# Kernel tuning notes

Measured on AMD Instinct MI355X. Metric: run time of the kernel, lower is better.

Reference implementation:

```python
import jax, jax.numpy as jnp
import numpy as np

B, L, DIM = 2, 4096, 512
HEADS, KS = 8, 33
HEAD_DIM = DIM // HEADS
SCALE = HEAD_DIM ** -0.5


def setup_inputs() -> dict:
    key = jax.random.key(0)
    ks = jax.random.split(key, 5)
    s = 0.02
    return {
        "x": jax.random.normal(ks[0], (B, L, DIM), dtype=jnp.float32),
        "w_qkv": jax.random.normal(ks[1], (3 * DIM, DIM), dtype=jnp.float32) * s,
        "b_qkv": jax.random.normal(ks[2], (3 * DIM,), dtype=jnp.float32) * s,
        "w_proj": jax.random.normal(ks[3], (DIM, DIM), dtype=jnp.float32) * s,
        "b_proj": jax.random.normal(ks[4], (DIM,), dtype=jnp.float32) * s,
    }


def _na1d(q, k, v):
    # q,k,v: [B, L, H, d]. Each query i attends to KS tokens whose window
    # start is clamp(i - KS//2, 0, L-KS) (NATTEN boundary-clamped neighborhood).
    starts = jnp.clip(jnp.arange(L) - KS // 2, 0, L - KS)          # [L]
    idx = starts[:, None] + jnp.arange(KS)[None, :]                # [L, KS]
    k_g = k[:, idx]                                                # [B, L, KS, H, d]
    v_g = v[:, idx]                                                # [B, L, KS, H, d]
    scores = jnp.einsum("blhd,blkhd->bhlk", q * SCALE, k_g)        # [B, H, L, KS]
    attn = jax.nn.softmax(scores, axis=-1)
    out = jnp.einsum("bhlk,blkhd->blhd", attn, v_g)                # [B, L, H, d]
    return out


def reference(x, w_qkv, b_qkv, w_proj, b_proj):
    qkv = x @ w_qkv.T + b_qkv                                      # [B, L, 3*DIM]
    qkv = qkv.reshape(B, L, 3, HEADS, HEAD_DIM)
    q, k, v = qkv[:, :, 0], qkv[:, :, 1], qkv[:, :, 2]
    out = _na1d(q, k, v).reshape(B, L, DIM)
    return out @ w_proj.T + b_proj
```

## Files before the change

kernel.cpp:

```cpp
#include <hip/hip_runtime.h>
#include <hip/hip_bf16.h>

#define B_ 2
#define L_ 4096
#define DIM_ 512
#define HEADS_ 8
#define HDIM_ 64
#define KS_ 33

typedef __bf16 bf16;
typedef __bf16 bf16x4 __attribute__((ext_vector_type(4)));
typedef __bf16 bf16x8 __attribute__((ext_vector_type(8)));
typedef float f32x4 __attribute__((ext_vector_type(4)));

typedef __attribute__((address_space(3))) void lds_void;
typedef __attribute__((address_space(1))) const void glb_void;

__device__ __forceinline__ void async_cp16(const bf16* g, bf16* l)
{
    __builtin_amdgcn_global_load_lds((glb_void*)g, (lds_void*)l, 16, 0, 0);
}

__global__ __launch_bounds__(256)
void cvt_all(const float* __restrict__ x,  const float* __restrict__ wq,
             const float* __restrict__ bq, const float* __restrict__ wp,
             const float* __restrict__ bp,
             bf16* __restrict__ xb,  bf16* __restrict__ wqb,
             bf16* __restrict__ bqb, bf16* __restrict__ wpb,
             bf16* __restrict__ bpb)
{
    const int blk = blockIdx.x;
    const float* src; bf16* dst; int n, base;
    if (blk < 2048)       { src = x;  dst = xb;  n = 4194304; base = blk; }
    else if (blk < 2432)  { src = wq; dst = wqb; n = 786432;  base = blk - 2048; }
    else if (blk < 2560)  { src = wp; dst = wpb; n = 262144;  base = blk - 2432; }
    else if (blk == 2560) { src = bq; dst = bqb; n = 1536;    base = 0; }
    else                  { src = bp; dst = bpb; n = 512;     base = 0; }
    int i = base * 2048 + threadIdx.x * 8;
    if (i + 8 <= n) {
        float4 a = *(const float4*)(src + i);
        float4 b = *(const float4*)(src + i + 4);
        bf16x8 o;
        o[0] = (bf16)a.x; o[1] = (bf16)a.y; o[2] = (bf16)a.z; o[3] = (bf16)a.w;
        o[4] = (bf16)b.x; o[5] = (bf16)b.y; o[6] = (bf16)b.z; o[7] = (bf16)b.w;
        *(bf16x8*)(dst + i) = o;
    }
}

template <typename OutT>
__global__ __launch_bounds__(256)
void gemm_nt_bias(const bf16* __restrict__ A, const bf16* __restrict__ W,
                  const bf16* __restrict__ bias, OutT* __restrict__ C,
                  int M, int N, int K)
{
    __shared__ bf16 As[128][64];
    __shared__ bf16 Bs[128][64];

    const int tid  = threadIdx.x;
    const int wave = tid >> 6;
    const int lane = tid & 63;
    const int wm   = (wave >> 1) * 64;
    const int wn   = (wave & 1) * 64;
    const int l16  = lane & 15;
    const int quad = lane >> 4;

    const int row0 = blockIdx.x * 128;
    const int col0 = blockIdx.y * 128;

    f32x4 acc[4][4] = {};

    for (int k0 = 0; k0 < K; k0 += 64) {
        #pragma unroll
        for (int it = 0; it < 4; ++it) {
            int f   = it * 256 + tid;
            int r   = f >> 3;
            int c8l = (f & 7) ^ (r & 7);
            async_cp16(&A[(size_t)(row0 + r) * K + k0 + c8l * 8], &As[r][(f & 7) * 8]);
            async_cp16(&W[(size_t)(col0 + r) * K + k0 + c8l * 8], &Bs[r][(f & 7) * 8]);
        }
        __syncthreads();

        #pragma unroll
        for (int ks = 0; ks < 2; ++ks) {
            bf16x8 af[4], bfr[4];
            #pragma unroll
            for (int i = 0; i < 4; ++i) {
                int ra = wm + i * 16 + l16;
                int rb = wn + i * 16 + l16;
                af[i]  = *(const bf16x8*)(&As[ra][((ks * 4 + quad) ^ (ra & 7)) * 8]);
                bfr[i] = *(const bf16x8*)(&Bs[rb][((ks * 4 + quad) ^ (rb & 7)) * 8]);
            }
            #pragma unroll
            for (int mi = 0; mi < 4; ++mi)
                #pragma unroll
                for (int ni = 0; ni < 4; ++ni)
                    acc[mi][ni] = __builtin_amdgcn_mfma_f32_16x16x32_bf16(
                        af[mi], bfr[ni], acc[mi][ni], 0, 0, 0);
        }
        __syncthreads();
    }

    #pragma unroll
    for (int ni = 0; ni < 4; ++ni) {
        int n = col0 + wn + ni * 16 + l16;
        float bv = (float)bias[n];
        #pragma unroll
        for (int mi = 0; mi < 4; ++mi) {
            int mrow = row0 + wm + mi * 16 + quad * 4;
            #pragma unroll
            for (int r = 0; r < 4; ++r)
                C[(size_t)(mrow + r) * N + n] = (OutT)(acc[mi][ni][r] + bv);
        }
    }
}

__global__ __launch_bounds__(256)
void na1d_attn_mfma(const bf16* __restrict__ qkv, bf16* __restrict__ att)
{
    __shared__ bf16 Klds[96 * 64];
    __shared__ bf16 Vlds[96 * 66];
    __shared__ bf16 Plds[4][16][72];

    const int tid  = threadIdx.x;
    const int wave = tid >> 6;
    const int lane = tid & 63;
    const int l16  = lane & 15;
    const int quad = lane >> 4;

    const int xcd  = blockIdx.x & 7;
    const int s    = blockIdx.x >> 3;
    const int jj   = s & 3;
    const int half = (s >> 2) & 1;
    const int h    = (s >> 3) & 7;
    const int b    = s >> 6;
    const int p    = jj * 8 + xcd;
    const int Q0   = p * 128 + half * 64;

    const size_t rs = 3 * DIM_;
    const size_t rowbase = (size_t)b * L_;

    #pragma unroll
    for (int i = 0; i < 3; ++i) {
        int ck = i * 256 + tid;
        int r  = ck >> 3;
        int pc = ck & 7;
        int lc = pc ^ (r & 7);
        int g  = Q0 - 16 + r;
        g = g < 0 ? 0 : (g > L_ - 1 ? L_ - 1 : g);
        async_cp16(qkv + (rowbase + g) * rs + DIM_ + h * HDIM_ + lc * 8,
                   Klds + (size_t)ck * 8);
    }
    {
        unsigned int* V32 = (unsigned int*)Vlds;
        #pragma unroll
        for (int i = 0; i < 3; ++i) {
            int cv = i * 256 + tid;
            int r  = cv >> 3;
            int pc = cv & 7;
            int g  = Q0 - 16 + r;
            g = g < 0 ? 0 : (g > L_ - 1 ? L_ - 1 : g);
            uint4 val = *(const uint4*)(qkv + (rowbase + g) * rs + 2 * DIM_ + h * HDIM_ + pc * 8);
            int base = r * 33 + pc * 4;
            V32[base + 0] = val.x; V32[base + 1] = val.y;
            V32[base + 2] = val.z; V32[base + 3] = val.w;
        }
    }

    const int q0w = Q0 + wave * 16;
    const bf16* qptr = qkv + (rowbase + q0w + l16) * rs + h * HDIM_ + quad * 8;
    bf16x8 qf0 = *(const bf16x8*)(qptr);
    bf16x8 qf1 = *(const bf16x8*)(qptr + 32);

    int k_base = q0w - 16;
    if (k_base > L_ - 48) k_base = L_ - 48;
    if (k_base < 0) k_base = 0;
    const int rel = k_base - (Q0 - 16);

    __syncthreads();

    f32x4 sacc[3] = {};
    #pragma unroll
    for (int t = 0; t < 3; ++t) {
        int r = rel + t * 16 + l16;
        bf16x8 kf0 = *(const bf16x8*)(Klds + r * 64 + ((quad ^ (r & 7)) * 8));
        bf16x8 kf1 = *(const bf16x8*)(Klds + r * 64 + (((4 + quad) ^ (r & 7)) * 8));
        sacc[t] = __builtin_amdgcn_mfma_f32_16x16x32_bf16(qf0, kf0, sacc[t], 0, 0, 0);
        sacc[t] = __builtin_amdgcn_mfma_f32_16x16x32_bf16(qf1, kf1, sacc[t], 0, 0, 0);
    }

    int offr[4];
    #pragma unroll
    for (int r = 0; r < 4; ++r) {
        int lq = q0w + quad * 4 + r;
        int st = lq - KS_ / 2;
        if (st < 0) st = 0;
        if (st > L_ - KS_) st = L_ - KS_;
        offr[r] = st - k_base;
    }
    float sv[3][4];
    #pragma unroll
    for (int t = 0; t < 3; ++t) {
        int j = t * 16 + l16;
        #pragma unroll
        for (int r = 0; r < 4; ++r) {
            float xv = sacc[t][r] * 0.125f;
            sv[t][r] = (j >= offr[r] && j <= offr[r] + 32) ? xv : -1e30f;
        }
    }

    float mr[4], sum[4];
    #pragma unroll
    for (int r = 0; r < 4; ++r)
        mr[r] = fmaxf(fmaxf(sv[0][r], sv[1][r]), sv[2][r]);
    #pragma unroll
    for (int o = 1; o < 16; o <<= 1)
        #pragma unroll
        for (int r = 0; r < 4; ++r)
            mr[r] = fmaxf(mr[r], __shfl_xor(mr[r], o, 64));
    #pragma unroll
    for (int t = 0; t < 3; ++t)
        #pragma unroll
        for (int r = 0; r < 4; ++r)
            sv[t][r] = __expf(sv[t][r] - mr[r]);
    #pragma unroll
    for (int r = 0; r < 4; ++r)
        sum[r] = sv[0][r] + sv[1][r] + sv[2][r];
    #pragma unroll
    for (int o = 1; o < 16; o <<= 1)
        #pragma unroll
        for (int r = 0; r < 4; ++r)
            sum[r] += __shfl_xor(sum[r], o, 64);
    #pragma unroll
    for (int r = 0; r < 4; ++r) {
        float inv = 1.0f / sum[r];
        #pragma unroll
        for (int t = 0; t < 3; ++t) sv[t][r] *= inv;
    }

    bf16* P = &Plds[wave][0][0];
    {
        int rr = lane >> 2;
        int c0 = 48 + (lane & 3) * 4;
        *(bf16x4*)(&P[rr * 72 + c0]) = (bf16x4){(bf16)0.f, (bf16)0.f, (bf16)0.f, (bf16)0.f};
    }
    #pragma unroll
    for (int t = 0; t < 3; ++t)
        #pragma unroll
        for (int r = 0; r < 4; ++r)
            P[(quad * 4 + r) * 72 + t * 16 + l16] = (bf16)sv[t][r];
    __syncthreads();

    bf16x8 pf0 = *(const bf16x8*)(&P[l16 * 72 + quad * 8]);
    bf16x8 pf1 = *(const bf16x8*)(&P[l16 * 72 + 32 + quad * 8]);

    f32x4 o[4] = {};
    #pragma unroll
    for (int t = 0; t < 4; ++t) {
        bf16x8 vf0, vf1;
        #pragma unroll
        for (int j = 0; j < 8; ++j) {
            vf0[j] = Vlds[(rel + quad * 8 + j) * 66 + t * 16 + l16];
            vf1[j] = Vlds[(rel + 32 + quad * 8 + j) * 66 + t * 16 + l16];
        }
        o[t] = __builtin_amdgcn_mfma_f32_16x16x32_bf16(pf0, vf0, o[t], 0, 0, 0);
        o[t] = __builtin_amdgcn_mfma_f32_16x16x32_bf16(pf1, vf1, o[t], 0, 0, 0);
    }

    bf16* orow = att + (rowbase + q0w) * DIM_ + h * HDIM_;
    #pragma unroll
    for (int t = 0; t < 4; ++t)
        #pragma unroll
        for (int r = 0; r < 4; ++r)
            orow[(size_t)(quad * 4 + r) * DIM_ + t * 16 + l16] = (bf16)o[t][r];
}

extern "C" void kernel_launch(void* const* d_in, const int* in_sizes, int n_in,
                              void* d_out, int out_size, void* d_ws, size_t ws_size,
                              hipStream_t stream) {
    const int n_x  = B_ * L_ * DIM_;
    const int n_wq = 3 * DIM_ * DIM_;
    const int n_bq = 3 * DIM_;
    const int n_wp = DIM_ * DIM_;
    const int n_bp = DIM_;

    char* ws = (char*)d_ws;
    bf16* xb  = (bf16*)ws;
    bf16* wqb = xb  + n_x;
    bf16* bqb = wqb + n_wq;
    bf16* wpb = bqb + n_bq;
    bf16* bpb = wpb + n_wp;
    bf16* qkv = bpb + n_bp;
    bf16* att = qkv + (size_t)8192 * 1536;

    float* out = (float*)d_out;
    const int M = B_ * L_;

    cvt_all<<<2562, 256, 0, stream>>>(
        (const float*)d_in[0], (const float*)d_in[1], (const float*)d_in[2],
        (const float*)d_in[3], (const float*)d_in[4],
        xb, wqb, bqb, wpb, bpb);

    gemm_nt_bias<bf16><<<dim3(M / 128, (3 * DIM_) / 128), 256, 0, stream>>>(
        xb, wqb, bqb, qkv, M, 3 * DIM_, DIM_);

    na1d_attn_mfma<<<dim3((B_ * HEADS_ * L_) / 64), 256, 0, stream>>>(qkv, att);

    gemm_nt_bias<float><<<dim3(M / 128, DIM_ / 128), 256, 0, stream>>>(
        att, wpb, bpb, out, M, DIM_, DIM_);
}
```

Measured before the change: 123.2 us.

## Store V transposed from QKV GEMM and load V fragments directly in attention

The QKV projection now gets its own kernel that writes Q and K to a packed [M,1024] buffer and V transposed to a [B, DIM, L] buffer. The attention kernel no longer stages V through LDS with scalar 16-bit gathers. Each lane instead loads contiguous 8-element bf16 vectors of V straight from global memory as the MFMA B operand, with a clamp to stay in bounds at the sequence end. The aim is to drop the LDS transpose and the many ds_read_u16 instructions. In exchange the GEMM epilogue does strided 8-byte stores for V, and attention relies on the cache for V reuse across waves.

```diff
diff --git a/kernel.cpp b/kernel.cpp
--- a/kernel.cpp
+++ b/kernel.cpp
@@ -7,6 +7,7 @@
 #define HEADS_ 8
 #define HDIM_ 64
 #define KS_ 33
+#define QKS_ 1024
 
 typedef __bf16 bf16;
 typedef __bf16 bf16x4 __attribute__((ext_vector_type(4)));
@@ -47,11 +48,10 @@
     }
 }
 
-template <typename OutT>
 __global__ __launch_bounds__(256)
-void gemm_nt_bias(const bf16* __restrict__ A, const bf16* __restrict__ W,
-                  const bf16* __restrict__ bias, OutT* __restrict__ C,
-                  int M, int N, int K)
+void gemm_qkv(const bf16* __restrict__ A, const bf16* __restrict__ W,
+              const bf16* __restrict__ bias,
+              bf16* __restrict__ qk, bf16* __restrict__ vT)
 {
     __shared__ bf16 As[128][64];
     __shared__ bf16 Bs[128][64];
@@ -66,6 +66,7 @@
 
     const int row0 = blockIdx.x * 128;
     const int col0 = blockIdx.y * 128;
+    const int K    = DIM_;
 
     f32x4 acc[4][4] = {};
 
@@ -100,6 +101,92 @@
         __syncthreads();
     }
 
+    if (col0 < 1024) {
+        #pragma unroll
+        for (int ni = 0; ni < 4; ++ni) {
+            int n = col0 + wn + ni * 16 + l16;
+            float bv = (float)bias[n];
+            #pragma unroll
+            for (int mi = 0; mi < 4; ++mi) {
+                int mrow = row0 + wm + mi * 16 + quad * 4;
+                #pragma unroll
+                for (int r = 0; r < 4; ++r)
+                    qk[(size_t)(mrow + r) * QKS_ + n] = (bf16)(acc[mi][ni][r] + bv);
+            }
+        }
+    } else {
+        #pragma unroll
+        for (int ni = 0; ni < 4; ++ni) {
+            int nf = col0 + wn + ni * 16 + l16;
+            float bv = (float)bias[nf];
+            int hd = nf - 1024;
+            #pragma unroll
+            for (int mi = 0; mi < 4; ++mi) {
+                int m = row0 + wm + mi * 16 + quad * 4;
+                int b = m >> 12;
+                int l = m & (L_ - 1);
+                bf16x4 v4;
+                #pragma unroll
+                for (int r = 0; r < 4; ++r) v4[r] = (bf16)(acc[mi][ni][r] + bv);
+                *(bf16x4*)(vT + ((size_t)(b * DIM_ + hd)) * L_ + l) = v4;
+            }
+        }
+    }
+}
+
+template <typename OutT>
+__global__ __launch_bounds__(256)
+void gemm_nt_bias(const bf16* __restrict__ A, const bf16* __restrict__ W,
+                  const bf16* __restrict__ bias, OutT* __restrict__ C,
+                  int M, int N, int K)
+{
+    __shared__ bf16 As[128][64];
+    __shared__ bf16 Bs[128][64];
+
+    const int tid  = threadIdx.x;
+    const int wave = tid >> 6;
+    const int lane = tid & 63;
+    const int wm   = (wave >> 1) * 64;
+    const int wn   = (wave & 1) * 64;
+    const int l16  = lane & 15;
+    const int quad = lane >> 4;
+
+    const int row0 = blockIdx.x * 128;
+    const int col0 = blockIdx.y * 128;
+
+    f32x4 acc[4][4] = {};
+
+    for (int k0 = 0; k0 < K; k0 += 64) {
+        #pragma unroll
+        for (int it = 0; it < 4; ++it) {
+            int f   = it * 256 + tid;
+            int r   = f >> 3;
+            int c8l = (f & 7) ^ (r & 7);
+            async_cp16(&A[(size_t)(row0 + r) * K + k0 + c8l * 8], &As[r][(f & 7) * 8]);
+            async_cp16(&W[(size_t)(col0 + r) * K + k0 + c8l * 8], &Bs[r][(f & 7) * 8]);
+        }
+        __syncthreads();
+
+        #pragma unroll
+        for (int ks = 0; ks < 2; ++ks) {
+            bf16x8 af[4], bfr[4];
+            #pragma unroll
+            for (int i = 0; i < 4; ++i) {
+                int ra = wm + i * 16 + l16;
+                int rb = wn + i * 16 + l16;
+                af[i]  = *(const bf16x8*)(&As[ra][((ks * 4 + quad) ^ (ra & 7)) * 8]);
+                bfr[i] = *(const bf16x8*)(&Bs[rb][((ks * 4 + quad) ^ (rb & 7)) * 8]);
+            }
+            #pragma unroll
+            for (int mi = 0; mi < 4; ++mi)
+                #pragma unroll
+                for (int ni = 0; ni < 4; ++ni)
+                    acc[mi][ni] = __builtin_amdgcn_mfma_f32_16x16x32_bf16(
+                        af[mi], bfr[ni], acc[mi][ni], 0, 0, 0);
+        }
+        __syncthreads();
+    }
+
     #pragma unroll
     for (int ni = 0; ni < 4; ++ni) {
         int n = col0 + wn + ni * 16 + l16;
@@ -115,10 +202,10 @@
 }
 
 __global__ __launch_bounds__(256)
-void na1d_attn_mfma(const bf16* __restrict__ qkv, bf16* __restrict__ att)
+void na1d_attn_mfma(const bf16* __restrict__ qk, const bf16* __restrict__ vT,
+                    bf16* __restrict__ att)
 {
     __shared__ bf16 Klds[96 * 64];
-    __shared__ bf16 Vlds[96 * 66];
     __shared__ bf16 Plds[4][16][72];
 
     const int tid  = threadIdx.x;
@@ -136,7 +223,6 @@
     const int p    = jj * 8 + xcd;
     const int Q0   = p * 128 + half * 64;
 
-    const size_t rs = 3 * DIM_;
     const size_t rowbase = (size_t)b * L_;
 
     #pragma unroll
@@ -147,27 +233,12 @@
         int lc = pc ^ (r & 7);
         int g  = Q0 - 16 + r;
         g = g < 0 ? 0 : (g > L_ - 1 ? L_ - 1 : g);
-        async_cp16(qkv + (rowbase + g) * rs + DIM_ + h * HDIM_ + lc * 8,
+        async_cp16(qk + (rowbase + g) * QKS_ + DIM_ + h * HDIM_ + lc * 8,
                    Klds + (size_t)ck * 8);
     }
-    {
-        unsigned int* V32 = (unsigned int*)Vlds;
-        #pragma unroll
-        for (int i = 0; i < 3; ++i) {
-            int cv = i * 256 + tid;
-            int r  = cv >> 3;
-            int pc = cv & 7;
-            int g  = Q0 - 16 + r;
-            g = g < 0 ? 0 : (g > L_ - 1 ? L_ - 1 : g);
-            uint4 val = *(const uint4*)(qkv + (rowbase + g) * rs + 2 * DIM_ + h * HDIM_ + pc * 8);
-            int base = r * 33 + pc * 4;
-            V32[base + 0] = val.x; V32[base + 1] = val.y;
-            V32[base + 2] = val.z; V32[base + 3] = val.w;
-        }
-    }
 
     const int q0w = Q0 + wave * 16;
-    const bf16* qptr = qkv + (rowbase + q0w + l16) * rs + h * HDIM_ + quad * 8;
+    const bf16* qptr = qk + (rowbase + q0w + l16) * QKS_ + h * HDIM_ + quad * 8;
     bf16x8 qf0 = *(const bf16x8*)(qptr);
     bf16x8 qf1 = *(const bf16x8*)(qptr + 32);
 
@@ -253,15 +324,16 @@
     bf16x8 pf0 = *(const bf16x8*)(&P[l16 * 72 + quad * 8]);
     bf16x8 pf1 = *(const bf16x8*)(&P[l16 * 72 + 32 + quad * 8]);
 
+    const bf16* vbase = vT + (size_t)(b * DIM_ + h * HDIM_) * L_;
+    int c1 = k_base + quad * 8;
+    int c2 = k_base + 32 + quad * 8;
+    if (c2 > L_ - 8) c2 = L_ - 8;
     f32x4 o[4] = {};
     #pragma unroll
     for (int t = 0; t < 4; ++t) {
-        bf16x8 vf0, vf1;
-        #pragma unroll
-        for (int j = 0; j < 8; ++j) {
-            vf0[j] = Vlds[(rel + quad * 8 + j) * 66 + t * 16 + l16];
-            vf1[j] = Vlds[(rel + 32 + quad * 8 + j) * 66 + t * 16 + l16];
-        }
+        const bf16* vrow = vbase + (size_t)(t * 16 + l16) * L_;
+        bf16x8 vf0 = *(const bf16x8*)(vrow + c1);
+        bf16x8 vf1 = *(const bf16x8*)(vrow + c2);
         o[t] = __builtin_amdgcn_mfma_f32_16x16x32_bf16(pf0, vf0, o[t], 0, 0, 0);
         o[t] = __builtin_amdgcn_mfma_f32_16x16x32_bf16(pf1, vf1, o[t], 0, 0, 0);
     }
@@ -289,8 +361,9 @@
     bf16* bqb = wqb + n_wq;
     bf16* wpb = bqb + n_bq;
     bf16* bpb = wpb + n_wp;
-    bf16* qkv = bpb + n_bp;
-    bf16* att = qkv + (size_t)8192 * 1536;
+    bf16* qk  = bpb + n_bp;
+    bf16* vT  = qk  + (size_t)8192 * 1024;
+    bf16* att = vT  + (size_t)B_ * DIM_ * L_;
 
     float* out = (float*)d_out;
     const int M = B_ * L_;
@@ -300,10 +373,10 @@
         (const float*)d_in[3], (const float*)d_in[4],
         xb, wqb, bqb, wpb, bpb);
 
-    gemm_nt_bias<bf16><<<dim3(M / 128, (3 * DIM_) / 128), 256, 0, stream>>>(
-        xb, wqb, bqb, qkv, M, 3 * DIM_, DIM_);
-
-    na1d_attn_mfma<<<dim3((B_ * HEADS_ * L_) / 64), 256, 0, stream>>>(qkv, att);
+    gemm_qkv<<<dim3(M / 128, (3 * DIM_) / 128), 256, 0, stream>>>(
+        xb, wqb, bqb, qk, vT);
+
+    na1d_attn_mfma<<<dim3((B_ * HEADS_ * L_) / 64), 256, 0, stream>>>(qk, vT, att);
 
     gemm_nt_bias<float><<<dim3(M / 128, DIM_ / 128), 256, 0, stream>>>(
         att, wpb, bpb, out, M, DIM_, DIM_);
```

After: 125.3 us. Within noise of the previous version (+1.7%).
